# Performance work log

Hardware: AMD Instinct MI355X
Metric: run time of the kernel (lower is better)

## Reference

```python
import jax, jax.numpy as jnp
import numpy as np

N_NODES = 100000
N_EDGES = 1600000
D_FEAT = 128
D_EMB = 128
ROUNDS = 4
M_OUT = 32
NUM_GRAPHS = 512


def setup_inputs() -> dict:
    key = jax.random.key(0)
    ks = jax.random.split(key, 12)
    x = jax.random.normal(ks[0], (N_NODES, D_FEAT), dtype=jnp.float32)
    edge_index = jax.random.randint(ks[1], (2, N_EDGES), 0, N_NODES, dtype=jnp.int32)
    batch = jnp.sort(jax.random.randint(ks[2], (N_NODES,), 0, NUM_GRAPHS, dtype=jnp.int32))
    s = 1.0 / np.sqrt(D_EMB)
    emb_W = jax.random.uniform(ks[3], (D_FEAT, D_EMB), minval=-s, maxval=s, dtype=jnp.float32)
    emb_b = jax.random.uniform(ks[4], (D_EMB,), minval=-s, maxval=s, dtype=jnp.float32)
    msg_W = jax.random.uniform(ks[5], (ROUNDS, D_EMB, D_EMB), minval=-s, maxval=s, dtype=jnp.float32)
    msg_b = jax.random.uniform(ks[6], (ROUNDS, D_EMB), minval=-s, maxval=s, dtype=jnp.float32)
    upd_W = jax.random.uniform(ks[7], (ROUNDS, D_EMB, D_EMB), minval=-s, maxval=s, dtype=jnp.float32)
    upd_b = jax.random.uniform(ks[8], (ROUNDS, D_EMB), minval=-s, maxval=s, dtype=jnp.float32)
    out_W = jax.random.uniform(ks[9], (D_EMB, M_OUT), minval=-s, maxval=s, dtype=jnp.float32)
    out_b = jax.random.uniform(ks[10], (M_OUT,), minval=-s, maxval=s, dtype=jnp.float32)
    return {"x": x, "edge_index": edge_index, "batch": batch,
            "emb_W": emb_W, "emb_b": emb_b, "msg_W": msg_W, "msg_b": msg_b,
            "upd_W": upd_W, "upd_b": upd_b, "out_W": out_W, "out_b": out_b}


def reference(x, edge_index, batch, emb_W, emb_b, msg_W, msg_b, upd_W, upd_b, out_W, out_b):
    src, dst = edge_index[0], edge_index[1]
    # initial node embedding: Linear + ReLU
    state = jax.nn.relu(x @ emb_W + emb_b)  # [N, D]
    for r in range(ROUNDS):
        message = jax.nn.relu(state @ msg_W[r] + msg_b[r])      # [N, D]
        # gather messages along edges, scatter-add to destination nodes
        aggregated = jax.ops.segment_sum(message[src], dst, num_segments=N_NODES)  # [N, D]
        state = state + jax.nn.relu(aggregated @ upd_W[r] + upd_b[r])
    # sum-pool nodes into graphs
    graph_state = jax.ops.segment_sum(state, batch, num_segments=NUM_GRAPHS)  # [G, D]
    return graph_state @ out_W + out_b  # [G, M]
```

## Files before the change

kernel.cpp:

```cpp
#include <hip/hip_runtime.h>

#define N_NODES    100000
#define N_EDGES    1600000
#define D_EMB      128
#define ROUNDS     4
#define M_OUT      32
#define NUM_GRAPHS 512

#define N_TILES    (N_NODES / 32)
#define GEMM_BLOCKS 1024

#define NPASS      8
#define PASS_RANGE (N_NODES / NPASS)

#define SCAN_ELEMS_PER_BLOCK 1024
#define SCAN_NBLK ((N_NODES + SCAN_ELEMS_PER_BLOCK - 1) / SCAN_ELEMS_PER_BLOCK)

typedef __attribute__((ext_vector_type(8))) short short8;
typedef __attribute__((ext_vector_type(4))) float f32x4;

static __device__ __forceinline__ unsigned short f2bf(float f) {
    union { float f; unsigned u; } v; v.f = f;
    unsigned u = v.u;
    unsigned r = (u + 0x7FFFu + ((u >> 16) & 1u)) >> 16;
    return (unsigned short)r;
}
static __device__ __forceinline__ float bf2f(unsigned short h) {
    union { unsigned u; float f; } v; v.u = ((unsigned)h) << 16;
    return v.f;
}

__global__ __launch_bounds__(256) void prep_weights_kernel(
    const float* __restrict__ emb_W, const float* __restrict__ msg_W,
    const float* __restrict__ upd_W, unsigned short* __restrict__ WTall)
{
    const int mi = blockIdx.x;
    const float* W = (mi == 0) ? emb_W
                   : (mi <= 4) ? msg_W + (size_t)(mi - 1) * D_EMB * D_EMB
                               : upd_W + (size_t)(mi - 5) * D_EMB * D_EMB;
    unsigned short* WT = WTall + (size_t)mi * D_EMB * D_EMB;
    for (int idx = threadIdx.x; idx < D_EMB * D_EMB; idx += 256) {
        const int n = idx >> 7, k = idx & 127;
        WT[idx] = f2bf(W[k * D_EMB + n]);
    }
}

template<int MODE, bool AF32>
__global__ __launch_bounds__(256) void gemm_loop_kernel(
    const void* __restrict__ Aptr, const unsigned short* __restrict__ WT,
    const float* __restrict__ bias, unsigned short* __restrict__ state,
    unsigned short* __restrict__ outb)
{
    __shared__ unsigned short As[2][32][136];

    const int tid  = threadIdx.x;
    const int lane = tid & 63;
    const int w    = tid >> 6;
    const int m    = lane & 15;
    const int g    = lane >> 4;

    short8 bfr[2][4];
    #pragma unroll
    for (int ct = 0; ct < 2; ++ct) {
        const int n = w * 32 + ct * 16 + m;
        #pragma unroll
        for (int ks = 0; ks < 4; ++ks)
            bfr[ct][ks] = *(const short8*)&WT[n * D_EMB + ks * 32 + g * 8];
    }
    const float bv0 = bias[w * 32 + m];
    const float bv1 = bias[w * 32 + 16 + m];

    int tile = blockIdx.x;

    if (AF32) {
        const float4* A4 = (const float4*)Aptr;
        #pragma unroll
        for (int i = 0; i < 4; ++i) {
            const int ch = tid + (i << 8);
            const float4 f = A4[(size_t)tile * 1024 + ch];
            ushort4 h; h.x = f2bf(f.x); h.y = f2bf(f.y); h.z = f2bf(f.z); h.w = f2bf(f.w);
            *(ushort4*)&As[0][ch >> 5][(ch & 31) << 2] = h;
        }
    } else {
        const uint4* A2 = (const uint4*)Aptr;
        #pragma unroll
        for (int i = 0; i < 2; ++i) {
            const int ch = tid + (i << 8);
            const uint4 v = A2[(size_t)tile * 512 + ch];
            *(uint4*)&As[0][ch >> 4][(ch & 15) << 3] = v;
        }
    }
    __syncthreads();

    int cur = 0;
    while (true) {
        const int next = tile + GEMM_BLOCKS;
        const bool have = next < N_TILES;

        float4 rgf[4]; uint4 rgu[2];
        if (have) {
            if (AF32) {
                const float4* A4 = (const float4*)Aptr;
                #pragma unroll
                for (int i = 0; i < 4; ++i)
                    rgf[i] = A4[(size_t)next * 1024 + tid + (i << 8)];
            } else {
                const uint4* A2 = (const uint4*)Aptr;
                #pragma unroll
                for (int i = 0; i < 2; ++i)
                    rgu[i] = A2[(size_t)next * 512 + tid + (i << 8)];
            }
        }

        short8 a[2][4];
        #pragma unroll
        for (int rt = 0; rt < 2; ++rt)
            #pragma unroll
            for (int ks = 0; ks < 4; ++ks)
                a[rt][ks] = *(const short8*)&As[cur][rt * 16 + m][ks * 32 + g * 8];

        f32x4 acc[2][2] = {};
        #pragma unroll
        for (int ks = 0; ks < 4; ++ks)
            #pragma unroll
            for (int rt = 0; rt < 2; ++rt)
                #pragma unroll
                for (int ct = 0; ct < 2; ++ct)
                    acc[rt][ct] = __builtin_amdgcn_mfma_f32_16x16x32_bf16(
                        a[rt][ks], bfr[ct][ks], acc[rt][ct], 0, 0, 0);

        if (have) {
            if (AF32) {
                #pragma unroll
                for (int i = 0; i < 4; ++i) {
                    const int ch = tid + (i << 8);
                    ushort4 h;
                    h.x = f2bf(rgf[i].x); h.y = f2bf(rgf[i].y);
                    h.z = f2bf(rgf[i].z); h.w = f2bf(rgf[i].w);
                    *(ushort4*)&As[cur ^ 1][ch >> 5][(ch & 31) << 2] = h;
                }
            } else {
                #pragma unroll
                for (int i = 0; i < 2; ++i) {
                    const int ch = tid + (i << 8);
                    *(uint4*)&As[cur ^ 1][ch >> 4][(ch & 15) << 3] = rgu[i];
                }
            }
        }

        #pragma unroll
        for (int rt = 0; rt < 2; ++rt) {
            #pragma unroll
            for (int ct = 0; ct < 2; ++ct) {
                const int col = w * 32 + ct * 16 + m;
                const float bv = ct ? bv1 : bv0;
                #pragma unroll
                for (int r = 0; r < 4; ++r) {
                    const int row = tile * 32 + rt * 16 + g * 4 + r;
                    const size_t idx = (size_t)row * D_EMB + col;
                    const float v = fmaxf(acc[rt][ct][r] + bv, 0.f);
                    if (MODE == 0) outb[idx] = f2bf(v);
                    else           state[idx] = f2bf(v);
                }
            }
        }

        if (!have) break;
        __syncthreads();
        cur ^= 1;
        tile = next;
    }
}

__global__ __launch_bounds__(256) void hist_mp_kernel(
    const int* __restrict__ dst, int* __restrict__ deg)
{
    const int p = blockIdx.x & 7;
    const int e = (blockIdx.x >> 3) * 256 + threadIdx.x;
    const int d = dst[e];
    if ((unsigned)(d - p * PASS_RANGE) < (unsigned)PASS_RANGE)
        atomicAdd(&deg[d], 1);
}

__global__ __launch_bounds__(256) void scan_local_kernel(
    const int* __restrict__ deg, int* __restrict__ rp, int* __restrict__ partials)
{
    __shared__ int sm[256];
    const int tid  = threadIdx.x;
    const int base = blockIdx.x * SCAN_ELEMS_PER_BLOCK + tid * 4;

    int v0 = (base + 0 < N_NODES) ? deg[base + 0] : 0;
    int v1 = (base + 1 < N_NODES) ? deg[base + 1] : 0;
    int v2 = (base + 2 < N_NODES) ? deg[base + 2] : 0;
    int v3 = (base + 3 < N_NODES) ? deg[base + 3] : 0;
    const int tot = v0 + v1 + v2 + v3;

    sm[tid] = tot;
    __syncthreads();
    #pragma unroll
    for (int off = 1; off < 256; off <<= 1) {
        const int x = (tid >= off) ? sm[tid - off] : 0;
        __syncthreads();
        sm[tid] += x;
        __syncthreads();
    }
    const int bex = sm[tid] - tot;

    if (base + 0 < N_NODES) rp[base + 0] = bex;
    if (base + 1 < N_NODES) rp[base + 1] = bex + v0;
    if (base + 2 < N_NODES) rp[base + 2] = bex + v0 + v1;
    if (base + 3 < N_NODES) rp[base + 3] = bex + v0 + v1 + v2;
    if (tid == 255) partials[blockIdx.x] = sm[255];
}

__global__ __launch_bounds__(128) void scan_partials_kernel(int* __restrict__ partials)
{
    __shared__ int sm[128];
    const int tid = threadIdx.x;
    const int v = (tid < SCAN_NBLK) ? partials[tid] : 0;
    sm[tid] = v;
    __syncthreads();
    #pragma unroll
    for (int off = 1; off < 128; off <<= 1) {
        const int x = (tid >= off) ? sm[tid - off] : 0;
        __syncthreads();
        sm[tid] += x;
        __syncthreads();
    }
    if (tid < SCAN_NBLK) partials[tid] = sm[tid] - v;
}

__global__ __launch_bounds__(256) void scan_fixup_kernel(
    int* __restrict__ rp, const int* __restrict__ partials, int* __restrict__ pos)
{
    const int i = blockIdx.x * 256 + threadIdx.x;
    if (i < N_NODES) {
        const int v = rp[i] + partials[i >> 10];
        rp[i] = v;
        pos[i] = v;
    }
    if (i == 0) rp[N_NODES] = N_EDGES;
}

__global__ __launch_bounds__(256) void fill_mp_kernel(
    const int* __restrict__ src, const int* __restrict__ dst,
    int* __restrict__ pos, int* __restrict__ esrc)
{
    const int p = blockIdx.x & 7;
    const int e = (blockIdx.x >> 3) * 256 + threadIdx.x;
    const int d = dst[e];
    if ((unsigned)(d - p * PASS_RANGE) < (unsigned)PASS_RANGE) {
        const int idx = atomicAdd(&pos[d], 1);
        esrc[idx] = src[e];
    }
}

__global__ __launch_bounds__(256) void fused_upd_kernel(
    const unsigned short* __restrict__ msg, const int* __restrict__ rp,
    const int* __restrict__ esrc, const unsigned short* __restrict__ WT,
    const float* __restrict__ bias, unsigned short* __restrict__ state)
{
    __shared__ unsigned short As[32][136];
    __shared__ int wq;

    const int tid  = threadIdx.x;
    const int lane = tid & 63;
    const int wid  = tid >> 6;
    const int m    = lane & 15;
    const int g    = lane >> 4;
    const int b    = blockIdx.x;
    const int j    = tid & 15;

    if (tid == 0) wq = 0;

    short8 bfr[2][4];
    #pragma unroll
    for (int ct = 0; ct < 2; ++ct) {
        const int n = wid * 32 + ct * 16 + m;
        #pragma unroll
        for (int ks = 0; ks < 4; ++ks)
            bfr[ct][ks] = *(const short8*)&WT[n * D_EMB + ks * 32 + g * 8];
    }
    const float bv0 = bias[wid * 32 + m];
    const float bv1 = bias[wid * 32 + 16 + m];

    __syncthreads();

    const uint4* m4 = (const uint4*)msg;

    while (true) {
        int t = 0;
        if (j == 0) t = atomicAdd(&wq, 1);
        t = __shfl(t, lane & 48, 64);
        if (t >= 32) break;

        const int n = b * 32 + t;
        const int beg = rp[n];
        const int end = rp[n + 1];

        float a0[8] = {0,0,0,0,0,0,0,0};
        float a1[8] = {0,0,0,0,0,0,0,0};
        int i = beg;
        for (; i + 3 < end; i += 4) {
            const uint4 v0 = m4[(size_t)esrc[i]     * 16 + j];
            const uint4 v1 = m4[(size_t)esrc[i + 1] * 16 + j];
            const uint4 v2 = m4[(size_t)esrc[i + 2] * 16 + j];
            const uint4 v3 = m4[(size_t)esrc[i + 3] * 16 + j];
            a0[0] += bf2f(v0.x & 0xffff); a0[1] += bf2f(v0.x >> 16);
            a0[2] += bf2f(v0.y & 0xffff); a0[3] += bf2f(v0.y >> 16);
            a0[4] += bf2f(v0.z & 0xffff); a0[5] += bf2f(v0.z >> 16);
            a0[6] += bf2f(v0.w & 0xffff); a0[7] += bf2f(v0.w >> 16);
            a1[0] += bf2f(v1.x & 0xffff); a1[1] += bf2f(v1.x >> 16);
            a1[2] += bf2f(v1.y & 0xffff); a1[3] += bf2f(v1.y >> 16);
            a1[4] += bf2f(v1.z & 0xffff); a1[5] += bf2f(v1.z >> 16);
            a1[6] += bf2f(v1.w & 0xffff); a1[7] += bf2f(v1.w >> 16);
            a0[0] += bf2f(v2.x & 0xffff); a0[1] += bf2f(v2.x >> 16);
            a0[2] += bf2f(v2.y & 0xffff); a0[3] += bf2f(v2.y >> 16);
            a0[4] += bf2f(v2.z & 0xffff); a0[5] += bf2f(v2.z >> 16);
            a0[6] += bf2f(v2.w & 0xffff); a0[7] += bf2f(v2.w >> 16);
            a1[0] += bf2f(v3.x & 0xffff); a1[1] += bf2f(v3.x >> 16);
            a1[2] += bf2f(v3.y & 0xffff); a1[3] += bf2f(v3.y >> 16);
            a1[4] += bf2f(v3.z & 0xffff); a1[5] += bf2f(v3.z >> 16);
            a1[6] += bf2f(v3.w & 0xffff); a1[7] += bf2f(v3.w >> 16);
        }
        for (; i < end; ++i) {
            const uint4 v0 = m4[(size_t)esrc[i] * 16 + j];
            a0[0] += bf2f(v0.x & 0xffff); a0[1] += bf2f(v0.x >> 16);
            a0[2] += bf2f(v0.y & 0xffff); a0[3] += bf2f(v0.y >> 16);
            a0[4] += bf2f(v0.z & 0xffff); a0[5] += bf2f(v0.z >> 16);
            a0[6] += bf2f(v0.w & 0xffff); a0[7] += bf2f(v0.w >> 16);
        }
        #pragma unroll
        for (int q = 0; q < 8; ++q) a0[q] += a1[q];

        uint4 o;
        o.x = (unsigned)f2bf(a0[0]) | ((unsigned)f2bf(a0[1]) << 16);
        o.y = (unsigned)f2bf(a0[2]) | ((unsigned)f2bf(a0[3]) << 16);
        o.z = (unsigned)f2bf(a0[4]) | ((unsigned)f2bf(a0[5]) << 16);
        o.w = (unsigned)f2bf(a0[6]) | ((unsigned)f2bf(a0[7]) << 16);
        *(uint4*)&As[t][j * 8] = o;
    }
    __syncthreads();

    short8 a[2][4];
    #pragma unroll
    for (int rt = 0; rt < 2; ++rt)
        #pragma unroll
        for (int ks = 0; ks < 4; ++ks)
            a[rt][ks] = *(const short8*)&As[rt * 16 + m][ks * 32 + g * 8];

    f32x4 acc[2][2] = {};
    #pragma unroll
    for (int ks = 0; ks < 4; ++ks)
        #pragma unroll
        for (int rt = 0; rt < 2; ++rt)
            #pragma unroll
            for (int ct = 0; ct < 2; ++ct)
                acc[rt][ct] = __builtin_amdgcn_mfma_f32_16x16x32_bf16(
                    a[rt][ks], bfr[ct][ks], acc[rt][ct], 0, 0, 0);

    #pragma unroll
    for (int rt = 0; rt < 2; ++rt) {
        #pragma unroll
        for (int ct = 0; ct < 2; ++ct) {
            const int col = wid * 32 + ct * 16 + m;
            const float bv = ct ? bv1 : bv0;
            #pragma unroll
            for (int r = 0; r < 4; ++r) {
                const int row = b * 32 + rt * 16 + g * 4 + r;
                const size_t idx = (size_t)row * D_EMB + col;
                const float v = fmaxf(acc[rt][ct][r] + bv, 0.f);
                state[idx] = f2bf(bf2f(state[idx]) + v);
            }
        }
    }
}

__global__ __launch_bounds__(256) void pool_kernel(
    const unsigned short* __restrict__ state, const int* __restrict__ batch,
    float* __restrict__ gs)
{
    const int lane = threadIdx.x & 63;
    const int grp  = threadIdx.x >> 6;
    const int n0 = blockIdx.x * 128 + grp * 32;
    const int c0 = lane * 2;

    float a0 = 0.f, a1 = 0.f;
    int cur = -1;
    for (int i = 0; i < 32; ++i) {
        const int n = n0 + i;
        if (n >= N_NODES) break;
        const int bb = batch[n];
        if (bb != cur) {
            if (cur >= 0) {
                unsafeAtomicAdd(&gs[cur * D_EMB + c0],     a0);
                unsafeAtomicAdd(&gs[cur * D_EMB + c0 + 1], a1);
            }
            cur = bb; a0 = 0.f; a1 = 0.f;
        }
        const unsigned u = *(const unsigned*)&state[(size_t)n * D_EMB + c0];
        a0 += bf2f(u & 0xffff);
        a1 += bf2f(u >> 16);
    }
    if (cur >= 0) {
        unsafeAtomicAdd(&gs[cur * D_EMB + c0],     a0);
        unsafeAtomicAdd(&gs[cur * D_EMB + c0 + 1], a1);
    }
}

__global__ __launch_bounds__(256) void out_kernel(
    const float* __restrict__ gs, const float* __restrict__ W,
    const float* __restrict__ bias, float* __restrict__ out)
{
    const int idx = blockIdx.x * 256 + threadIdx.x;
    const int g = idx >> 5;
    const int m = idx & 31;
    float acc = 0.f;
    #pragma unroll 8
    for (int k = 0; k < D_EMB; ++k)
        acc += gs[g * D_EMB + k] * W[k * M_OUT + m];
    out[idx] = acc + bias[m];
}

extern "C" void kernel_launch(void* const* d_in, const int* in_sizes, int n_in,
                              void* d_out, int out_size, void* d_ws, size_t ws_size,
                              hipStream_t stream)
{
    const float* x     = (const float*)d_in[0];
    const int*   eidx  = (const int*)d_in[1];
    const int*   batch = (const int*)d_in[2];
    const float* emb_W = (const float*)d_in[3];
    const float* emb_b = (const float*)d_in[4];
    const float* msg_W = (const float*)d_in[5];
    const float* msg_b = (const float*)d_in[6];
    const float* upd_W = (const float*)d_in[7];
    const float* upd_b = (const float*)d_in[8];
    const float* out_W = (const float*)d_in[9];
    const float* out_b = (const float*)d_in[10];
    float* out = (float*)d_out;

    const int* src = eidx;
    const int* dst = eidx + N_EDGES;

    char* p = (char*)d_ws;
    unsigned short* state = (unsigned short*)p;   p += (size_t)N_NODES * D_EMB * 2;
    unsigned short* msg   = (unsigned short*)p;   p += (size_t)N_NODES * D_EMB * 2;
    float* gs = (float*)p;                        p += (size_t)NUM_GRAPHS * D_EMB * 4;
    unsigned short* WTall = (unsigned short*)p;   p += (size_t)9 * D_EMB * D_EMB * 2;
    int* rp   = (int*)p;                          p += (size_t)(N_NODES + 1) * 4;
    int* deg  = (int*)p;                          p += (size_t)N_NODES * 4;
    int* pos  = (int*)p;                          p += (size_t)N_NODES * 4;
    int* partials = (int*)p;                      p += (size_t)128 * 4;
    int* esrc = (int*)p;                          p += (size_t)N_EDGES * 4;

    const dim3 blk(256);
    const int mp_grid = (N_EDGES / 256) * NPASS;

    prep_weights_kernel<<<9, blk, 0, stream>>>(emb_W, msg_W, upd_W, WTall);
    hipMemsetAsync(deg, 0, (size_t)N_NODES * sizeof(int), stream);
    hist_mp_kernel<<<mp_grid, blk, 0, stream>>>(dst, deg);
    scan_local_kernel<<<SCAN_NBLK, blk, 0, stream>>>(deg, rp, partials);
    scan_partials_kernel<<<1, 128, 0, stream>>>(partials);
    scan_fixup_kernel<<<(SCAN_NBLK * SCAN_ELEMS_PER_BLOCK) / 256, blk, 0, stream>>>(rp, partials, pos);
    fill_mp_kernel<<<mp_grid, blk, 0, stream>>>(src, dst, pos, esrc);

    gemm_loop_kernel<2, true><<<GEMM_BLOCKS, blk, 0, stream>>>(
        x, WTall, emb_b, state, nullptr);

    for (int r = 0; r < ROUNDS; ++r) {
        gemm_loop_kernel<0, false><<<GEMM_BLOCKS, blk, 0, stream>>>(
            state, WTall + (size_t)(1 + r) * D_EMB * D_EMB,
            msg_b + (size_t)r * D_EMB, nullptr, msg);
        fused_upd_kernel<<<N_TILES, blk, 0, stream>>>(
            msg, rp, esrc, WTall + (size_t)(5 + r) * D_EMB * D_EMB,
            upd_b + (size_t)r * D_EMB, state);
    }

    hipMemsetAsync(gs, 0, (size_t)NUM_GRAPHS * D_EMB * sizeof(float), stream);
    pool_kernel<<<(N_NODES + 127) / 128, blk, 0, stream>>>(state, batch, gs);
    out_kernel<<<(NUM_GRAPHS * M_OUT) / 256, blk, 0, stream>>>(gs, out_W, out_b, out);
}
```

Before: 599.9 us.

## Fuse next-round message GEMM into update kernel and embed+msg into one kernel

Removes the standalone message GEMM launches. The embedding kernel now also computes round-0 messages, and each update kernel computes the next round's messages from the freshly updated state tile it holds in shared memory. Messages ping-pong between two buffers so a round never overwrites messages still being gathered. This saves a full read of state per round plus several launches, at the cost of extra registers and LDS reuse in the update kernel. It also adds nontemporal loads in the CSR build kernels.

```diff
diff --git a/kernel.cpp b/kernel.cpp
--- a/kernel.cpp
+++ b/kernel.cpp
@@ -8,8 +8,6 @@
 #define NUM_GRAPHS 512
 
 #define N_TILES    (N_NODES / 32)
-#define GEMM_BLOCKS 1024
-
 #define NPASS      8
 #define PASS_RANGE (N_NODES / NPASS)
 
@@ -45,139 +43,12 @@
     }
 }
 
-template<int MODE, bool AF32>
-__global__ __launch_bounds__(256) void gemm_loop_kernel(
-    const void* __restrict__ Aptr, const unsigned short* __restrict__ WT,
-    const float* __restrict__ bias, unsigned short* __restrict__ state,
-    unsigned short* __restrict__ outb)
-{
-    __shared__ unsigned short As[2][32][136];
-
-    const int tid  = threadIdx.x;
-    const int lane = tid & 63;
-    const int w    = tid >> 6;
-    const int m    = lane & 15;
-    const int g    = lane >> 4;
-
-    short8 bfr[2][4];
-    #pragma unroll
-    for (int ct = 0; ct < 2; ++ct) {
-        const int n = w * 32 + ct * 16 + m;
-        #pragma unroll
-        for (int ks = 0; ks < 4; ++ks)
-            bfr[ct][ks] = *(const short8*)&WT[n * D_EMB + ks * 32 + g * 8];
-    }
-    const float bv0 = bias[w * 32 + m];
-    const float bv1 = bias[w * 32 + 16 + m];
-
-    int tile = blockIdx.x;
-
-    if (AF32) {
-        const float4* A4 = (const float4*)Aptr;
-        #pragma unroll
-        for (int i = 0; i < 4; ++i) {
-            const int ch = tid + (i << 8);
-            const float4 f = A4[(size_t)tile * 1024 + ch];
-            ushort4 h; h.x = f2bf(f.x); h.y = f2bf(f.y); h.z = f2bf(f.z); h.w = f2bf(f.w);
-            *(ushort4*)&As[0][ch >> 5][(ch & 31) << 2] = h;
-        }
-    } else {
-        const uint4* A2 = (const uint4*)Aptr;
-        #pragma unroll
-        for (int i = 0; i < 2; ++i) {
-            const int ch = tid + (i << 8);
-            const uint4 v = A2[(size_t)tile * 512 + ch];
-            *(uint4*)&As[0][ch >> 4][(ch & 15) << 3] = v;
-        }
-    }
-    __syncthreads();
-
-    int cur = 0;
-    while (true) {
-        const int next = tile + GEMM_BLOCKS;
-        const bool have = next < N_TILES;
-
-        float4 rgf[4]; uint4 rgu[2];
-        if (have) {
-            if (AF32) {
-                const float4* A4 = (const float4*)Aptr;
-                #pragma unroll
-                for (int i = 0; i < 4; ++i)
-                    rgf[i] = A4[(size_t)next * 1024 + tid + (i << 8)];
-            } else {
-                const uint4* A2 = (const uint4*)Aptr;
-                #pragma unroll
-                for (int i = 0; i < 2; ++i)
-                    rgu[i] = A2[(size_t)next * 512 + tid + (i << 8)];
-            }
-        }
-
-        short8 a[2][4];
-        #pragma unroll
-        for (int rt = 0; rt < 2; ++rt)
-            #pragma unroll
-            for (int ks = 0; ks < 4; ++ks)
-                a[rt][ks] = *(const short8*)&As[cur][rt * 16 + m][ks * 32 + g * 8];
-
-        f32x4 acc[2][2] = {};
-        #pragma unroll
-        for (int ks = 0; ks < 4; ++ks)
-            #pragma unroll
-            for (int rt = 0; rt < 2; ++rt)
-                #pragma unroll
-                for (int ct = 0; ct < 2; ++ct)
-                    acc[rt][ct] = __builtin_amdgcn_mfma_f32_16x16x32_bf16(
-                        a[rt][ks], bfr[ct][ks], acc[rt][ct], 0, 0, 0);
-
-        if (have) {
-            if (AF32) {
-                #pragma unroll
-                for (int i = 0; i < 4; ++i) {
-                    const int ch = tid + (i << 8);
-                    ushort4 h;
-                    h.x = f2bf(rgf[i].x); h.y = f2bf(rgf[i].y);
-                    h.z = f2bf(rgf[i].z); h.w = f2bf(rgf[i].w);
-                    *(ushort4*)&As[cur ^ 1][ch >> 5][(ch & 31) << 2] = h;
-                }
-            } else {
-                #pragma unroll
-                for (int i = 0; i < 2; ++i) {
-                    const int ch = tid + (i << 8);
-                    *(uint4*)&As[cur ^ 1][ch >> 4][(ch & 15) << 3] = rgu[i];
-                }
-            }
-        }
-
-        #pragma unroll
-        for (int rt = 0; rt < 2; ++rt) {
-            #pragma unroll
-            for (int ct = 0; ct < 2; ++ct) {
-                const int col = w * 32 + ct * 16 + m;
-                const float bv = ct ? bv1 : bv0;
-                #pragma unroll
-                for (int r = 0; r < 4; ++r) {
-                    const int row = tile * 32 + rt * 16 + g * 4 + r;
-                    const size_t idx = (size_t)row * D_EMB + col;
-                    const float v = fmaxf(acc[rt][ct][r] + bv, 0.f);
-                    if (MODE == 0) outb[idx] = f2bf(v);
-                    else           state[idx] = f2bf(v);
-                }
-            }
-        }
-
-        if (!have) break;
-        __syncthreads();
-        cur ^= 1;
-        tile = next;
-    }
-}
-
 __global__ __launch_bounds__(256) void hist_mp_kernel(
     const int* __restrict__ dst, int* __restrict__ deg)
 {
     const int p = blockIdx.x & 7;
     const int e = (blockIdx.x >> 3) * 256 + threadIdx.x;
-    const int d = dst[e];
+    const int d = __builtin_nontemporal_load(&dst[e]);
     if ((unsigned)(d - p * PASS_RANGE) < (unsigned)PASS_RANGE)
         atomicAdd(&deg[d], 1);
 }
@@ -248,17 +119,137 @@
 {
     const int p = blockIdx.x & 7;
     const int e = (blockIdx.x >> 3) * 256 + threadIdx.x;
-    const int d = dst[e];
+    const int d = __builtin_nontemporal_load(&dst[e]);
     if ((unsigned)(d - p * PASS_RANGE) < (unsigned)PASS_RANGE) {
+        const int s = __builtin_nontemporal_load(&src[e]);
         const int idx = atomicAdd(&pos[d], 1);
-        esrc[idx] = src[e];
-    }
-}
-
+        esrc[idx] = s;
+    }
+}
+
+__global__ __launch_bounds__(256) void emb_msg_kernel(
+    const float* __restrict__ x,
+    const unsigned short* __restrict__ WTe, const float* __restrict__ eb,
+    const unsigned short* __restrict__ WTm, const float* __restrict__ mb,
+    unsigned short* __restrict__ state, unsigned short* __restrict__ msg)
+{
+    __shared__ unsigned short As[32][136];
+
+    const int tid  = threadIdx.x;
+    const int lane = tid & 63;
+    const int wid  = tid >> 6;
+    const int m    = lane & 15;
+    const int g    = lane >> 4;
+    const int tile = blockIdx.x;
+
+    const float4* A4 = (const float4*)x;
+    #pragma unroll
+    for (int i = 0; i < 4; ++i) {
+        const int ch = tid + (i << 8);
+        const float4 f = A4[(size_t)tile * 1024 + ch];
+        ushort4 h; h.x = f2bf(f.x); h.y = f2bf(f.y); h.z = f2bf(f.z); h.w = f2bf(f.w);
+        *(ushort4*)&As[ch >> 5][(ch & 31) << 2] = h;
+    }
+
+    short8 bfrE[2][4];
+    #pragma unroll
+    for (int ct = 0; ct < 2; ++ct) {
+        const int n = wid * 32 + ct * 16 + m;
+        #pragma unroll
+        for (int ks = 0; ks < 4; ++ks)
+            bfrE[ct][ks] = *(const short8*)&WTe[n * D_EMB + ks * 32 + g * 8];
+    }
+    const float ebv0 = eb[wid * 32 + m];
+    const float ebv1 = eb[wid * 32 + 16 + m];
+
+    __syncthreads();
+
+    short8 a[2][4];
+    #pragma unroll
+    for (int rt = 0; rt < 2; ++rt)
+        #pragma unroll
+        for (int ks = 0; ks < 4; ++ks)
+            a[rt][ks] = *(const short8*)&As[rt * 16 + m][ks * 32 + g * 8];
+    __syncthreads();
+
+    f32x4 acc[2][2] = {};
+    #pragma unroll
+    for (int ks = 0; ks < 4; ++ks)
+        #pragma unroll
+        for (int rt = 0; rt < 2; ++rt)
+            #pragma unroll
+            for (int ct = 0; ct < 2; ++ct)
+                acc[rt][ct] = __builtin_amdgcn_mfma_f32_16x16x32_bf16(
+                    a[rt][ks], bfrE[ct][ks], acc[rt][ct], 0, 0, 0);
+
+    #pragma unroll
+    for (int rt = 0; rt < 2; ++rt) {
+        #pragma unroll
+        for (int ct = 0; ct < 2; ++ct) {
+            const int col = wid * 32 + ct * 16 + m;
+            const float bv = ct ? ebv1 : ebv0;
+            #pragma unroll
+            for (int r = 0; r < 4; ++r) {
+                const int rl = rt * 16 + g * 4 + r;
+                const float v = fmaxf(acc[rt][ct][r] + bv, 0.f);
+                const unsigned short h = f2bf(v);
+                state[(size_t)(tile * 32 + rl) * D_EMB + col] = h;
+                As[rl][col] = h;
+            }
+        }
+    }
+    __syncthreads();
+
+    short8 bfrM[2][4];
+    #pragma unroll
+    for (int ct = 0; ct < 2; ++ct) {
+        const int n = wid * 32 + ct * 16 + m;
+        #pragma unroll
+        for (int ks = 0; ks < 4; ++ks)
+            bfrM[ct][ks] = *(const short8*)&WTm[n * D_EMB + ks * 32 + g * 8];
+    }
+    const float mbv0 = mb[wid * 32 + m];
+    const float mbv1 = mb[wid * 32 + 16 + m];
+
+    short8 a2[2][4];
+    #pragma unroll
+    for (int rt = 0; rt < 2; ++rt)
+        #pragma unroll
+        for (int ks = 0; ks < 4; ++ks)
+            a2[rt][ks] = *(const short8*)&As[rt * 16 + m][ks * 32 + g * 8];
+
+    f32x4 acc2[2][2] = {};
+    #pragma unroll
+    for (int ks = 0; ks < 4; ++ks)
+        #pragma unroll
+        for (int rt = 0; rt < 2; ++rt)
+            #pragma unroll
+            for (int ct = 0; ct < 2; ++ct)
+                acc2[rt][ct] = __builtin_amdgcn_mfma_f32_16x16x32_bf16(
+                    a2[rt][ks], bfrM[ct][ks], acc2[rt][ct], 0, 0, 0);
+
+    #pragma unroll
+    for (int rt = 0; rt < 2; ++rt) {
+        #pragma unroll
+        for (int ct = 0; ct < 2; ++ct) {
+            const int col = wid * 32 + ct * 16 + m;
+            const float bv = ct ? mbv1 : mbv0;
+            #pragma unroll
+            for (int r = 0; r < 4; ++r) {
+                const int row = tile * 32 + rt * 16 + g * 4 + r;
+                msg[(size_t)row * D_EMB + col] = f2bf(fmaxf(acc2[rt][ct][r] + bv, 0.f));
+            }
+        }
+    }
+}
+
+template<bool HAS_MSG>
 __global__ __launch_bounds__(256) void fused_upd_kernel(
-    const unsigned short* __restrict__ msg, const int* __restrict__ rp,
-    const int* __restrict__ esrc, const unsigned short* __restrict__ WT,
-    const float* __restrict__ bias, unsigned short* __restrict__ state)
+    const unsigned short* __restrict__ msg_in, const int* __restrict__ rp,
+    const int* __restrict__ esrc,
+    const unsigned short* __restrict__ WTu, const float* __restrict__ ub,
+    const unsigned short* __restrict__ WTm, const float* __restrict__ mb,
+    unsigned short* __restrict__ state, unsigned short* __restrict__ msg_out)
 {
     __shared__ unsigned short As[32][136];
     __shared__ int wq;
@@ -273,20 +264,20 @@
 
     if (tid == 0) wq = 0;
 
-    short8 bfr[2][4];
+    short8 bfrU[2][4];
     #pragma unroll
     for (int ct = 0; ct < 2; ++ct) {
         const int n = wid * 32 + ct * 16 + m;
         #pragma unroll
         for (int ks = 0; ks < 4; ++ks)
-            bfr[ct][ks] = *(const short8*)&WT[n * D_EMB + ks * 32 + g * 8];
-    }
-    const float bv0 = bias[wid * 32 + m];
-    const float bv1 = bias[wid * 32 + 16 + m];
-
-    __syncthreads();
-
-    const uint4* m4 = (const uint4*)msg;
+            bfrU[ct][ks] = *(const short8*)&WTu[n * D_EMB + ks * 32 + g * 8];
+    }
+    const float ubv0 = ub[wid * 32 + m];
+    const float ubv1 = ub[wid * 32 + 16 + m];
+
+    __syncthreads();
+
+    const uint4* m4 = (const uint4*)msg_in;
 
     while (true) {
         int t = 0;
@@ -348,6 +339,7 @@
         #pragma unroll
         for (int ks = 0; ks < 4; ++ks)
             a[rt][ks] = *(const short8*)&As[rt * 16 + m][ks * 32 + g * 8];
+    __syncthreads();
 
     f32x4 acc[2][2] = {};
     #pragma unroll
@@ -357,20 +349,69 @@
             #pragma unroll
             for (int ct = 0; ct < 2; ++ct)
                 acc[rt][ct] = __builtin_amdgcn_mfma_f32_16x16x32_bf16(
-                    a[rt][ks], bfr[ct][ks], acc[rt][ct], 0, 0, 0);
+                    a[rt][ks], bfrU[ct][ks], acc[rt][ct], 0, 0, 0);
 
     #pragma unroll
     for (int rt = 0; rt < 2; ++rt) {
         #pragma unroll
         for (int ct = 0; ct < 2; ++ct) {
             const int col = wid * 32 + ct * 16 + m;
-            const float bv = ct ? bv1 : bv0;
+            const float bv = ct ? ubv1 : ubv0;
             #pragma unroll
             for (int r = 0; r < 4; ++r) {
-                const int row = b * 32 + rt * 16 + g * 4 + r;
-                const size_t idx = (size_t)row * D_EMB + col;
+                const int rl = rt * 16 + g * 4 + r;
+                const size_t idx = (size_t)(b * 32 + rl) * D_EMB + col;
                 const float v = fmaxf(acc[rt][ct][r] + bv, 0.f);
-                state[idx] = f2bf(bf2f(state[idx]) + v);
+                const unsigned short h = f2bf(bf2f(state[idx]) + v);
+                state[idx] = h;
+                if (HAS_MSG) As[rl][col] = h;
+            }
+        }
+    }
+
+    if (HAS_MSG) {
+        __syncthreads();
+
+        short8 bfrM[2][4];
+        #pragma unroll
+        for (int ct = 0; ct < 2; ++ct) {
+            const int n = wid * 32 + ct * 16 + m;
+            #pragma unroll
+            for (int ks = 0; ks < 4; ++ks)
+                bfrM[ct][ks] = *(const short8*)&WTm[n * D_EMB + ks * 32 + g * 8];
+        }
+        const float mbv0 = mb[wid * 32 + m];
+        const float mbv1 = mb[wid * 32 + 16 + m];
+
+        short8 a2[2][4];
+        #pragma unroll
+        for (int rt = 0; rt < 2; ++rt)
+            #pragma unroll
+            for (int ks = 0; ks < 4; ++ks)
+                a2[rt][ks] = *(const short8*)&As[rt * 16 + m][ks * 32 + g * 8];
+
+        f32x4 acc2[2][2] = {};
+        #pragma unroll
+        for (int ks = 0; ks < 4; ++ks)
+            #pragma unroll
+            for (int rt = 0; rt < 2; ++rt)
+                #pragma unroll
+                for (int ct = 0; ct < 2; ++ct)
+                    acc2[rt][ct] = __builtin_amdgcn_mfma_f32_16x16x32_bf16(
+                        a2[rt][ks], bfrM[ct][ks], acc2[rt][ct], 0, 0, 0);
+
+        #pragma unroll
+        for (int rt = 0; rt < 2; ++rt) {
+            #pragma unroll
+            for (int ct = 0; ct < 2; ++ct) {
+                const int col = wid * 32 + ct * 16 + m;
+                const float bv = ct ? mbv1 : mbv0;
+                #pragma unroll
+                for (int r = 0; r < 4; ++r) {
+                    const int row = b * 32 + rt * 16 + g * 4 + r;
+                    msg_out[(size_t)row * D_EMB + col] =
+                        f2bf(fmaxf(acc2[rt][ct][r] + bv, 0.f));
+                }
             }
         }
     }
@@ -444,7 +485,8 @@
 
     char* p = (char*)d_ws;
     unsigned short* state = (unsigned short*)p;   p += (size_t)N_NODES * D_EMB * 2;
-    unsigned short* msg   = (unsigned short*)p;   p += (size_t)N_NODES * D_EMB * 2;
+    unsigned short* msgA  = (unsigned short*)p;   p += (size_t)N_NODES * D_EMB * 2;
+    unsigned short* msgB  = (unsigned short*)p;   p += (size_t)N_NODES * D_EMB * 2;
     float* gs = (float*)p;                        p += (size_t)NUM_GRAPHS * D_EMB * 4;
     unsigned short* WTall = (unsigned short*)p;   p += (size_t)9 * D_EMB * D_EMB * 2;
     int* rp   = (int*)p;                          p += (size_t)(N_NODES + 1) * 4;
@@ -464,16 +506,24 @@
     scan_fixup_kernel<<<(SCAN_NBLK * SCAN_ELEMS_PER_BLOCK) / 256, blk, 0, stream>>>(rp, partials, pos);
     fill_mp_kernel<<<mp_grid, blk, 0, stream>>>(src, dst, pos, esrc);
 
-    gemm_loop_kernel<2, true><<<GEMM_BLOCKS, blk, 0, stream>>>(
-        x, WTall, emb_b, state, nullptr);
-
+    emb_msg_kernel<<<N_TILES, blk, 0, stream>>>(
+        x, WTall, emb_b, WTall + (size_t)1 * D_EMB * D_EMB, msg_b, state, msgA);
+
+    unsigned short* mi = msgA;
+    unsigned short* mo = msgB;
     for (int r = 0; r < ROUNDS; ++r) {
-        gemm_loop_kernel<0, false><<<GEMM_BLOCKS, blk, 0, stream>>>(
-            state, WTall + (size_t)(1 + r) * D_EMB * D_EMB,
-            msg_b + (size_t)r * D_EMB, nullptr, msg);
-        fused_upd_kernel<<<N_TILES, blk, 0, stream>>>(
-            msg, rp, esrc, WTall + (size_t)(5 + r) * D_EMB * D_EMB,
-            upd_b + (size_t)r * D_EMB, state);
+        const unsigned short* WTu = WTall + (size_t)(5 + r) * D_EMB * D_EMB;
+        const float* ub = upd_b + (size_t)r * D_EMB;
+        if (r < ROUNDS - 1) {
+            const unsigned short* WTm = WTall + (size_t)(2 + r) * D_EMB * D_EMB;
+            const float* mb = msg_b + (size_t)(r + 1) * D_EMB;
+            fused_upd_kernel<true><<<N_TILES, blk, 0, stream>>>(
+                mi, rp, esrc, WTu, ub, WTm, mb, state, mo);
+        } else {
+            fused_upd_kernel<false><<<N_TILES, blk, 0, stream>>>(
+                mi, rp, esrc, WTu, ub, nullptr, nullptr, state, nullptr);
+        }
+        unsigned short* t = mi; mi = mo; mo = t;
     }
 
     hipMemsetAsync(gs, 0, (size_t)NUM_GRAPHS * D_EMB * sizeof(float), stream);
```

After: 603.5 us. Within noise of the previous version (+0.6%).
